# Kernel optimization log

Measured on AMD Instinct MI355X. Metric: run time of the kernel, lower is better.

Reference implementation:

```python
import jax, jax.numpy as jnp
import numpy as np

B, T, I, R, O = 64, 2048, 25, 512, 50
ALPHA = 0.5
RHO = 0.99


def setup_inputs() -> dict:
    key = jax.random.key(0)
    k1, k2, k3, k4 = jax.random.split(key, 4)
    x = jax.random.normal(k1, (B, T, I), dtype=jnp.float32)
    Win = jax.random.uniform(k2, (R, I), minval=-0.1, maxval=0.1, dtype=jnp.float32)
    W = jax.random.normal(k3, (R, R), dtype=jnp.float32) * 0.1
    sr_actual = np.max(np.abs(np.linalg.eigvals(np.asarray(W))))
    W = W / jnp.float32(sr_actual) * jnp.float32(RHO)
    Wout = jax.random.normal(k4, (O, R), dtype=jnp.float32) * 0.1
    return {"x": x, "Win": Win, "W": W, "Wout": Wout}


def reference(x, Win, W, Wout):
    a = jnp.asarray(ALPHA, dtype=x.dtype)
    # Precompute input projections for all timesteps (batched GEMM).
    xin = jnp.einsum('bti,ri->btr', x, Win)  # [B, T, R]

    def step(h, u):
        # h: [B, R], u: [B, R]
        h = (1 - a) * h + a * jnp.tanh(u + h @ W.T)
        return h, h

    h0 = jnp.zeros((x.shape[0], W.shape[0]), dtype=x.dtype)
    _, states = jax.lax.scan(step, h0, jnp.swapaxes(xin, 0, 1))  # [T, B, R]
    states = jnp.swapaxes(states, 0, 1)  # [B, T, R]
    return states @ Wout.T  # [B, T, O]
```

## Files before the change

### kernel.cpp

```cpp
#include <hip/hip_runtime.h>
#include <math.h>


typedef float v2f __attribute__((ext_vector_type(2)));
typedef float v4f __attribute__((ext_vector_type(4)));

template<int CTRL>
__device__ __forceinline__ float dpp_add(float x) {
    int y = __builtin_amdgcn_update_dpp(0, __float_as_int(x), CTRL, 0xF, 0xF, false);
    return x + __int_as_float(y);
}

__device__ __forceinline__ void store_ic8(float* p, float h, int tag) {
    v2f v; v[0] = h; v[1] = __int_as_float(tag);
    asm volatile("global_store_dwordx2 %0, %1, off sc0 sc1"
                 :: "v"(p), "v"(v) : "memory");
}
__device__ __forceinline__ void load3_ic(const float* p0, const float* p1,
                                         const float* p2, v4f& a, v4f& b, v4f& c) {
    asm volatile("global_load_dwordx4 %0, %3, off sc0 sc1\n\t"
                 "global_load_dwordx4 %1, %4, off sc0 sc1\n\t"
                 "global_load_dwordx4 %2, %5, off sc0 sc1\n\t"
                 "s_waitcnt vmcnt(0)"
                 : "=&v"(a), "=&v"(b), "=&v"(c)
                 : "v"(p0), "v"(p1), "v"(p2) : "memory");
}
__device__ __forceinline__ void load3_l2(const float* p0, const float* p1,
                                         const float* p2, v4f& a, v4f& b, v4f& c) {
    asm volatile("global_load_dwordx4 %0, %3, off sc0\n\t"
                 "global_load_dwordx4 %1, %4, off sc0\n\t"
                 "global_load_dwordx4 %2, %5, off sc0\n\t"
                 "s_waitcnt vmcnt(0)"
                 : "=&v"(a), "=&v"(b), "=&v"(c)
                 : "v"(p0), "v"(p1), "v"(p2) : "memory");
}

__device__ __forceinline__ int permidx(int c) {
    return (c >> 7) * 128 + (c & 31) * 4 + ((c >> 5) & 3);
}

#define TAGS_BAD (__any((__float_as_int(d0.y) != want) | (__float_as_int(d0.w) != want) | \
                        (__float_as_int(d1.y) != want) | (__float_as_int(d1.w) != want) | \
                        (__float_as_int(d2.y) != want) | (__float_as_int(d2.w) != want)))

__global__ void __launch_bounds__(512, 2)
esn_kernel(const float* __restrict__ x, const float* __restrict__ Win,
           const float* __restrict__ W, const float* __restrict__ Wout,
           float* __restrict__ out, float* __restrict__ Hf)
{
    const int b    = blockIdx.x & 63;
    const int g    = blockIdx.x >> 6;
    const int tid  = threadIdx.x;
    const int rt   = tid >> 5;
    const int ct   = tid & 31;
    const int lane = tid & 63;
    const int wv   = tid >> 6;
    const int hw   = rt & 1;

    __shared__ __align__(16) float hperm[2][512];

    v2f Wreg[64];
    {
        const int i0 = g*128 + rt*8;
        #pragma unroll
        for (int r = 0; r < 4; ++r)
        #pragma unroll
        for (int q = 0; q < 4; ++q) {
            const float* wp = W + (r*128 + q*32 + ct);
            #pragma unroll
            for (int p = 0; p < 4; ++p) {
                v2f w;
                w[0] = wp[(size_t)(i0 + 2*p    ) * 512];
                w[1] = wp[(size_t)(i0 + 2*p + 1) * 512];
                Wreg[(r*4+q)*4 + p] = w;
            }
        }
    }

    const int myrow = g*128 + rt*8 + (ct & 7);
    float WinR[25];
    #pragma unroll
    for (int k = 0; k < 25; ++k) WinR[k] = Win[myrow*25 + k];

    const int obase = g*13;
    const int ocnt  = (g == 3) ? 11 : 13;
    const int oloc  = 2*wv + hw;
    const bool ovalid = (oloc < ocnt);
    const int oidx  = obase + (ovalid ? oloc : 0);
    float WoutR[16];
    #pragma unroll
    for (int r = 0; r < 4; ++r)
    #pragma unroll
    for (int q = 0; q < 4; ++q)
        WoutR[r*4+q] = ovalid ? Wout[oidx*512 + r*128 + q*32 + ct] : 0.f;

    hperm[0][tid] = 0.f;
    float holdv = 0.f;
    const bool fin = (ct >= 16) & (ct < 24);

    const float* xrow = x   + (size_t)b * 2048 * 25;
    float*       orow = out + (size_t)b * 2048 * 50;
    float* HfB0 = Hf + (size_t)b * 1024;
    const int s0 = (g+1)&3, s1 = (g+2)&3, s2 = (g+3)&3;

    bool fast = true;

    __syncthreads();

    float u = 0.f;
    #pragma unroll
    for (int k = 0; k < 25; ++k) u = fmaf(WinR[k], xrow[k], u);

    for (int t = 0; t < 2048; ++t) {
        const int par  = t & 1;
        const int npar = par ^ 1;
        const int want = t + 1;
        float* HfN = HfB0 + (size_t)npar * 64 * 1024;

        v2f acc0 = {0.f,0.f}, acc1 = {0.f,0.f}, acc2 = {0.f,0.f}, acc3 = {0.f,0.f};
        float op = 0.f;
        #pragma unroll
        for (int r = 0; r < 4; ++r) {
            v4f hv = *(const v4f*)&hperm[par][r*128 + ct*4];
            #pragma unroll
            for (int q = 0; q < 4; ++q) {
                const float hs = hv[q];
                op = fmaf(WoutR[r*4+q], hs, op);
                v2f hh = {hs, hs};
                acc0 = __builtin_elementwise_fma(Wreg[(r*4+q)*4+0], hh, acc0);
                acc1 = __builtin_elementwise_fma(Wreg[(r*4+q)*4+1], hh, acc1);
                acc2 = __builtin_elementwise_fma(Wreg[(r*4+q)*4+2], hh, acc2);
                acc3 = __builtin_elementwise_fma(Wreg[(r*4+q)*4+3], hh, acc3);
            }
        }

        float ar[8] = {acc0[0],acc0[1],acc1[0],acc1[1],acc2[0],acc2[1],acc3[0],acc3[1]};
        #pragma unroll
        for (int j = 0; j < 8; ++j) {
            ar[j] = dpp_add<0xB1>(ar[j]);
            ar[j] = dpp_add<0x4E>(ar[j]);
            ar[j] = dpp_add<0x124>(ar[j]);
            ar[j] = dpp_add<0x128>(ar[j]);
            ar[j] = dpp_add<0x142>(ar[j]);
        }

        if (fin) {
            const int j = ct & 7;
            float y = ar[0];
            if (j == 1) y = ar[1];
            if (j == 2) y = ar[2];
            if (j == 3) y = ar[3];
            if (j == 4) y = ar[4];
            if (j == 5) y = ar[5];
            if (j == 6) y = ar[6];
            if (j == 7) y = ar[7];
            const float z  = u + y;
            const float e  = __expf(2.f * z);
            const float th = 1.f - 2.f * __builtin_amdgcn_rcpf(e + 1.f);
            holdv = 0.5f * holdv + 0.5f * th;
            hperm[npar][permidx(myrow)] = holdv;
            store_ic8(&HfN[myrow*2], holdv, want);
        }

        op = dpp_add<0xB1>(op);  op = dpp_add<0x4E>(op);
        op = dpp_add<0x124>(op); op = dpp_add<0x128>(op);
        op = dpp_add<0x142>(op);
        if (t > 0 && ovalid && ((lane & 31) == 31))
            orow[(size_t)(t-1)*50 + oidx] = op;
        {
            const int tt = (t < 2047) ? t + 1 : 2047;
            float un = 0.f;
            #pragma unroll
            for (int k = 0; k < 25; ++k) un = fmaf(WinR[k], xrow[tt*25 + k], un);
            u = un;
        }

        if (wv == 0) {
            const float* p0 = HfN + (s0*256 + lane*4);
            const float* p1 = HfN + (s1*256 + lane*4);
            const float* p2 = HfN + (s2*256 + lane*4);
            v4f d0, d1, d2;
            if (fast) {
                int tries = 0;
                do { load3_l2(p0, p1, p2, d0, d1, d2); } while (TAGS_BAD && ++tries < 64);
                if (TAGS_BAD) fast = false;
            }
            if (!fast) {
                do { load3_ic(p0, p1, p2, d0, d1, d2); } while (TAGS_BAD);
            }
            const int c0 = s0*128 + 2*lane, c1 = s1*128 + 2*lane, c2 = s2*128 + 2*lane;
            hperm[npar][permidx(c0)]     = d0.x;
            hperm[npar][permidx(c0 + 1)] = d0.z;
            hperm[npar][permidx(c1)]     = d1.x;
            hperm[npar][permidx(c1 + 1)] = d1.z;
            hperm[npar][permidx(c2)]     = d2.x;
            hperm[npar][permidx(c2 + 1)] = d2.z;
        }
        __syncthreads();
    }

    {
        float op = 0.f;
        #pragma unroll
        for (int r = 0; r < 4; ++r) {
            v4f hv = *(const v4f*)&hperm[0][r*128 + ct*4];
            #pragma unroll
            for (int q = 0; q < 4; ++q) op = fmaf(WoutR[r*4+q], hv[q], op);
        }
        op = dpp_add<0xB1>(op);  op = dpp_add<0x4E>(op);
        op = dpp_add<0x124>(op); op = dpp_add<0x128>(op);
        op = dpp_add<0x142>(op);
        if (ovalid && ((lane & 31) == 31))
            orow[(size_t)2047*50 + oidx] = op;
    }
}

extern "C" void kernel_launch(void* const* d_in, const int* in_sizes, int n_in,
                              void* d_out, int out_size, void* d_ws, size_t ws_size,
                              hipStream_t stream)
{
    (void)in_sizes; (void)n_in; (void)out_size; (void)ws_size;
    const float* x    = (const float*)d_in[0];
    const float* Win  = (const float*)d_in[1];
    const float* W    = (const float*)d_in[2];
    const float* Wout = (const float*)d_in[3];
    float* out = (float*)d_out;
    float* Hf  = (float*)d_ws;
    esn_kernel<<<dim3(256), dim3(512), 0, stream>>>(x, Win, W, Wout, out, Hf);
}
```

Baseline: 2.757 ms.

## Split recurrence across 8 blocks per pair of batches instead of 4 per batch

Each block now owns 64 reservoir rows (not 128) for two batch elements at once, so each batch's hidden state is spread over 8 blocks. This halves per-thread W register use and FMA work per step. In exchange, each step must gather 7 remote slices per batch through tagged global-memory flags instead of 3. The dependent chains of the two batches are interleaved to hide latency, and the first step gets a larger spin budget before falling back to the slower uncached polling path.

```diff
diff --git a/kernel.cpp b/kernel.cpp
--- a/kernel.cpp
+++ b/kernel.cpp
@@ -10,46 +10,126 @@
     int y = __builtin_amdgcn_update_dpp(0, __float_as_int(x), CTRL, 0xF, 0xF, false);
     return x + __int_as_float(y);
 }
+#define DPP_REDUCE32(v) do { v = dpp_add<0xB1>(v); v = dpp_add<0x4E>(v); \
+    v = dpp_add<0x124>(v); v = dpp_add<0x128>(v); v = dpp_add<0x142>(v); } while (0)
 
 __device__ __forceinline__ void store_ic8(float* p, float h, int tag) {
     v2f v; v[0] = h; v[1] = __int_as_float(tag);
     asm volatile("global_store_dwordx2 %0, %1, off sc0 sc1"
                  :: "v"(p), "v"(v) : "memory");
 }
-__device__ __forceinline__ void load3_ic(const float* p0, const float* p1,
-                                         const float* p2, v4f& a, v4f& b, v4f& c) {
-    asm volatile("global_load_dwordx4 %0, %3, off sc0 sc1\n\t"
-                 "global_load_dwordx4 %1, %4, off sc0 sc1\n\t"
-                 "global_load_dwordx4 %2, %5, off sc0 sc1\n\t"
-                 "s_waitcnt vmcnt(0)"
-                 : "=&v"(a), "=&v"(b), "=&v"(c)
-                 : "v"(p0), "v"(p1), "v"(p2) : "memory");
-}
-__device__ __forceinline__ void load3_l2(const float* p0, const float* p1,
-                                         const float* p2, v4f& a, v4f& b, v4f& c) {
-    asm volatile("global_load_dwordx4 %0, %3, off sc0\n\t"
-                 "global_load_dwordx4 %1, %4, off sc0\n\t"
-                 "global_load_dwordx4 %2, %5, off sc0\n\t"
-                 "s_waitcnt vmcnt(0)"
-                 : "=&v"(a), "=&v"(b), "=&v"(c)
-                 : "v"(p0), "v"(p1), "v"(p2) : "memory");
+
+__device__ __forceinline__ void load7_l2(
+    const float* p0, const float* p1, const float* p2, const float* p3,
+    const float* p4, const float* p5, const float* p6,
+    v2f& d0, v2f& d1, v2f& d2, v2f& d3, v2f& d4, v2f& d5, v2f& d6)
+{
+    asm volatile(
+        "global_load_dwordx2 %0, %7, off sc0\n\t"
+        "global_load_dwordx2 %1, %8, off sc0\n\t"
+        "global_load_dwordx2 %2, %9, off sc0\n\t"
+        "global_load_dwordx2 %3, %10, off sc0\n\t"
+        "global_load_dwordx2 %4, %11, off sc0\n\t"
+        "global_load_dwordx2 %5, %12, off sc0\n\t"
+        "global_load_dwordx2 %6, %13, off sc0\n\t"
+        "s_waitcnt vmcnt(0)"
+        : "=&v"(d0), "=&v"(d1), "=&v"(d2), "=&v"(d3), "=&v"(d4), "=&v"(d5), "=&v"(d6)
+        : "v"(p0), "v"(p1), "v"(p2), "v"(p3), "v"(p4), "v"(p5), "v"(p6)
+        : "memory");
+}
+__device__ __forceinline__ void load7_ic(
+    const float* p0, const float* p1, const float* p2, const float* p3,
+    const float* p4, const float* p5, const float* p6,
+    v2f& d0, v2f& d1, v2f& d2, v2f& d3, v2f& d4, v2f& d5, v2f& d6)
+{
+    asm volatile(
+        "global_load_dwordx2 %0, %7, off sc0 sc1\n\t"
+        "global_load_dwordx2 %1, %8, off sc0 sc1\n\t"
+        "global_load_dwordx2 %2, %9, off sc0 sc1\n\t"
+        "global_load_dwordx2 %3, %10, off sc0 sc1\n\t"
+        "global_load_dwordx2 %4, %11, off sc0 sc1\n\t"
+        "global_load_dwordx2 %5, %12, off sc0 sc1\n\t"
+        "global_load_dwordx2 %6, %13, off sc0 sc1\n\t"
+        "s_waitcnt vmcnt(0)"
+        : "=&v"(d0), "=&v"(d1), "=&v"(d2), "=&v"(d3), "=&v"(d4), "=&v"(d5), "=&v"(d6)
+        : "v"(p0), "v"(p1), "v"(p2), "v"(p3), "v"(p4), "v"(p5), "v"(p6)
+        : "memory");
 }
 
 __device__ __forceinline__ int permidx(int c) {
     return (c >> 7) * 128 + (c & 31) * 4 + ((c >> 5) & 3);
 }
 
-#define TAGS_BAD (__any((__float_as_int(d0.y) != want) | (__float_as_int(d0.w) != want) | \
-                        (__float_as_int(d1.y) != want) | (__float_as_int(d1.w) != want) | \
-                        (__float_as_int(d2.y) != want) | (__float_as_int(d2.w) != want)))
+#define TAGS_BAD (__any((__float_as_int(d0.y) != want) | (__float_as_int(d1.y) != want) | \
+                        (__float_as_int(d2.y) != want) | (__float_as_int(d3.y) != want) | \
+                        (__float_as_int(d4.y) != want) | (__float_as_int(d5.y) != want) | \
+                        (__float_as_int(d6.y) != want)))
+
+#define CHAIN_COMPUTE(c, uvar, holdvar, orowp, hfN) do {                      \
+    v2f acc0 = {0.f,0.f}, acc1 = {0.f,0.f};                                   \
+    float op = 0.f;                                                           \
+    _Pragma("unroll")                                                         \
+    for (int r = 0; r < 4; ++r) {                                             \
+        v4f hv = *(const v4f*)&hperm[c][par][r*128 + ct*4];                   \
+        _Pragma("unroll")                                                     \
+        for (int q = 0; q < 4; ++q) {                                         \
+            const float hs = hv[q];                                           \
+            op = fmaf(WoutR[r*4+q], hs, op);                                  \
+            v2f hh = {hs, hs};                                                \
+            acc0 = __builtin_elementwise_fma(Wreg[(r*4+q)*2+0], hh, acc0);    \
+            acc1 = __builtin_elementwise_fma(Wreg[(r*4+q)*2+1], hh, acc1);    \
+        }                                                                     \
+    }                                                                         \
+    float a0 = acc0[0], a1 = acc0[1], a2 = acc1[0], a3 = acc1[1];             \
+    DPP_REDUCE32(a0); DPP_REDUCE32(a1); DPP_REDUCE32(a2); DPP_REDUCE32(a3);   \
+    if (fin) {                                                                \
+        const int j = ct & 3;                                                 \
+        float y = a0;                                                         \
+        if (j == 1) y = a1;                                                   \
+        if (j == 2) y = a2;                                                   \
+        if (j == 3) y = a3;                                                   \
+        const float z  = uvar + y;                                            \
+        const float e  = __expf(2.f * z);                                     \
+        const float th = 1.f - 2.f * __builtin_amdgcn_rcpf(e + 1.f);          \
+        holdvar = 0.5f * holdvar + 0.5f * th;                                 \
+        hperm[c][npar][pmyrow] = holdvar;                                     \
+        store_ic8((hfN) + 2*myrow, holdvar, want);        \
+    }                                                                         \
+                          \
+    DPP_REDUCE32(op);                                                         \
+    if (t > 0 && ovalid && ((lane & 31) == 31))                               \
+        (orowp)[(size_t)(t-1)*50 + oidx] = op;                                \
+} while (0)
+
+#define U_NEXT(uvar, xrowp) do {                                              \
+    const int tt = (t < 2047) ? t + 1 : 2047;                                 \
+    float un = 0.f;                                                           \
+    _Pragma("unroll")                                                         \
+    for (int k = 0; k < 25; ++k) un = fmaf(WinR[k], (xrowp)[tt*25 + k], un);  \
+    uvar = un;                                                                \
+} while (0)
+
+#define CHAIN_EPI(c, orowp) do {                                              \
+    float op = 0.f;                                                           \
+    _Pragma("unroll")                                                         \
+    for (int r = 0; r < 4; ++r) {                                             \
+        v4f hv = *(const v4f*)&hperm[c][0][r*128 + ct*4];                     \
+        _Pragma("unroll")                                                     \
+        for (int q = 0; q < 4; ++q) op = fmaf(WoutR[r*4+q], hv[q], op);       \
+    }                                                                         \
+    DPP_REDUCE32(op);                                                         \
+    if (ovalid && ((lane & 31) == 31))                                        \
+        (orowp)[(size_t)2047*50 + oidx] = op;                                 \
+} while (0)
 
 __global__ void __launch_bounds__(512, 2)
 esn_kernel(const float* __restrict__ x, const float* __restrict__ Win,
            const float* __restrict__ W, const float* __restrict__ Wout,
            float* __restrict__ out, float* __restrict__ Hf)
 {
-    const int b    = blockIdx.x & 63;
-    const int g    = blockIdx.x >> 6;
+    const int p    = blockIdx.x & 31;
+    const int g    = blockIdx.x >> 5;
+    const int b0   = 2*p, b1 = 2*p + 1;
     const int tid  = threadIdx.x;
     const int rt   = tid >> 5;
     const int ct   = tid & 31;
@@ -57,33 +137,34 @@
     const int wv   = tid >> 6;
     const int hw   = rt & 1;
 
-    __shared__ __align__(16) float hperm[2][512];
-
-    v2f Wreg[64];
+    __shared__ __align__(16) float hperm[2][2][512];
+
+    v2f Wreg[32];
     {
-        const int i0 = g*128 + rt*8;
+        const int i0 = g*64 + rt*4;
         #pragma unroll
         for (int r = 0; r < 4; ++r)
         #pragma unroll
         for (int q = 0; q < 4; ++q) {
             const float* wp = W + (r*128 + q*32 + ct);
             #pragma unroll
-            for (int p = 0; p < 4; ++p) {
+            for (int pp = 0; pp < 2; ++pp) {
                 v2f w;
-                w[0] = wp[(size_t)(i0 + 2*p    ) * 512];
-                w[1] = wp[(size_t)(i0 + 2*p + 1) * 512];
-                Wreg[(r*4+q)*4 + p] = w;
+                w[0] = wp[(size_t)(i0 + 2*pp    ) * 512];
+                w[1] = wp[(size_t)(i0 + 2*pp + 1) * 512];
+                Wreg[(r*4+q)*2 + pp] = w;
             }
         }
     }
 
-    const int myrow = g*128 + rt*8 + (ct & 7);
+    const int myrow  = g*64 + rt*4 + (ct & 3);
+    const int pmyrow = permidx(myrow);
     float WinR[25];
     #pragma unroll
     for (int k = 0; k < 25; ++k) WinR[k] = Win[myrow*25 + k];
 
-    const int obase = g*13;
-    const int ocnt  = (g == 3) ? 11 : 13;
+    const int obase = g*7;
+    const int ocnt  = (g == 7) ? 1 : 7;
     const int oloc  = 2*wv + hw;
     const bool ovalid = (oloc < ocnt);
     const int oidx  = obase + (ovalid ? oloc : 0);
@@ -94,125 +175,77 @@
     for (int q = 0; q < 4; ++q)
         WoutR[r*4+q] = ovalid ? Wout[oidx*512 + r*128 + q*32 + ct] : 0.f;
 
-    hperm[0][tid] = 0.f;
-    float holdv = 0.f;
-    const bool fin = (ct >= 16) & (ct < 24);
-
-    const float* xrow = x   + (size_t)b * 2048 * 25;
-    float*       orow = out + (size_t)b * 2048 * 50;
-    float* HfB0 = Hf + (size_t)b * 1024;
-    const int s0 = (g+1)&3, s1 = (g+2)&3, s2 = (g+3)&3;
+    hperm[0][0][tid] = 0.f;
+    hperm[1][0][tid] = 0.f;
+    float holdv0 = 0.f, holdv1 = 0.f;
+    const bool fin = (ct >= 16) & (ct < 20);
+
+    const float* xrow0 = x   + (size_t)b0 * 2048 * 25;
+    const float* xrow1 = x   + (size_t)b1 * 2048 * 25;
+    float*       orow0 = out + (size_t)b0 * 2048 * 50;
+    float*       orow1 = out + (size_t)b1 * 2048 * 50;
+    float* HfB0 = Hf + (size_t)b0 * 1024;
+    float* HfB1 = Hf + (size_t)b1 * 1024;
+
+    const int s0=(g+1)&7, s1=(g+2)&7, s2=(g+3)&7, s3=(g+4)&7,
+              s4=(g+5)&7, s5=(g+6)&7, s6=(g+7)&7;
+    const int o0 = s0*128 + lane*2, o1 = s1*128 + lane*2, o2 = s2*128 + lane*2,
+              o3 = s3*128 + lane*2, o4 = s4*128 + lane*2, o5 = s5*128 + lane*2,
+              o6 = s6*128 + lane*2;
+    const int pi0 = permidx(s0*64 + lane), pi1 = permidx(s1*64 + lane),
+              pi2 = permidx(s2*64 + lane), pi3 = permidx(s3*64 + lane),
+              pi4 = permidx(s4*64 + lane), pi5 = permidx(s5*64 + lane),
+              pi6 = permidx(s6*64 + lane);
 
     bool fast = true;
 
     __syncthreads();
 
-    float u = 0.f;
-    #pragma unroll
-    for (int k = 0; k < 25; ++k) u = fmaf(WinR[k], xrow[k], u);
+    float u0 = 0.f, u1 = 0.f;
+    #pragma unroll
+    for (int k = 0; k < 25; ++k) u0 = fmaf(WinR[k], xrow0[k], u0);
+    #pragma unroll
+    for (int k = 0; k < 25; ++k) u1 = fmaf(WinR[k], xrow1[k], u1);
 
     for (int t = 0; t < 2048; ++t) {
         const int par  = t & 1;
         const int npar = par ^ 1;
         const int want = t + 1;
-        float* HfN = HfB0 + (size_t)npar * 64 * 1024;
-
-        v2f acc0 = {0.f,0.f}, acc1 = {0.f,0.f}, acc2 = {0.f,0.f}, acc3 = {0.f,0.f};
-        float op = 0.f;
-        #pragma unroll
-        for (int r = 0; r < 4; ++r) {
-            v4f hv = *(const v4f*)&hperm[par][r*128 + ct*4];
-            #pragma unroll
-            for (int q = 0; q < 4; ++q) {
-                const float hs = hv[q];
-                op = fmaf(WoutR[r*4+q], hs, op);
-                v2f hh = {hs, hs};
-                acc0 = __builtin_elementwise_fma(Wreg[(r*4+q)*4+0], hh, acc0);
-                acc1 = __builtin_elementwise_fma(Wreg[(r*4+q)*4+1], hh, acc1);
-                acc2 = __builtin_elementwise_fma(Wreg[(r*4+q)*4+2], hh, acc2);
-                acc3 = __builtin_elementwise_fma(Wreg[(r*4+q)*4+3], hh, acc3);
-            }
-        }
-
-        float ar[8] = {acc0[0],acc0[1],acc1[0],acc1[1],acc2[0],acc2[1],acc3[0],acc3[1]};
-        #pragma unroll
-        for (int j = 0; j < 8; ++j) {
-            ar[j] = dpp_add<0xB1>(ar[j]);
-            ar[j] = dpp_add<0x4E>(ar[j]);
-            ar[j] = dpp_add<0x124>(ar[j]);
-            ar[j] = dpp_add<0x128>(ar[j]);
-            ar[j] = dpp_add<0x142>(ar[j]);
-        }
-
-        if (fin) {
-            const int j = ct & 7;
-            float y = ar[0];
-            if (j == 1) y = ar[1];
-            if (j == 2) y = ar[2];
-            if (j == 3) y = ar[3];
-            if (j == 4) y = ar[4];
-            if (j == 5) y = ar[5];
-            if (j == 6) y = ar[6];
-            if (j == 7) y = ar[7];
-            const float z  = u + y;
-            const float e  = __expf(2.f * z);
-            const float th = 1.f - 2.f * __builtin_amdgcn_rcpf(e + 1.f);
-            holdv = 0.5f * holdv + 0.5f * th;
-            hperm[npar][permidx(myrow)] = holdv;
-            store_ic8(&HfN[myrow*2], holdv, want);
-        }
-
-        op = dpp_add<0xB1>(op);  op = dpp_add<0x4E>(op);
-        op = dpp_add<0x124>(op); op = dpp_add<0x128>(op);
-        op = dpp_add<0x142>(op);
-        if (t > 0 && ovalid && ((lane & 31) == 31))
-            orow[(size_t)(t-1)*50 + oidx] = op;
-        {
-            const int tt = (t < 2047) ? t + 1 : 2047;
-            float un = 0.f;
-            #pragma unroll
-            for (int k = 0; k < 25; ++k) un = fmaf(WinR[k], xrow[tt*25 + k], un);
-            u = un;
-        }
-
-        if (wv == 0) {
-            const float* p0 = HfN + (s0*256 + lane*4);
-            const float* p1 = HfN + (s1*256 + lane*4);
-            const float* p2 = HfN + (s2*256 + lane*4);
-            v4f d0, d1, d2;
+        float* HfN0 = HfB0 + (size_t)npar * 65536;
+        float* HfN1 = HfB1 + (size_t)npar * 65536;
+
+        CHAIN_COMPUTE(0, u0, holdv0, orow0, HfN0);
+        U_NEXT(u0, xrow0);
+        CHAIN_COMPUTE(1, u1, holdv1, orow1, HfN1);
+        U_NEXT(u1, xrow1);
+
+        if (wv < 2) {
+            float* HfN = wv ? HfN1 : HfN0;
+            const float* q0 = HfN + o0; const float* q1 = HfN + o1;
+            const float* q2 = HfN + o2; const float* q3 = HfN + o3;
+            const float* q4 = HfN + o4; const float* q5 = HfN + o5;
+            const float* q6 = HfN + o6;
+            v2f d0, d1, d2, d3, d4, d5, d6;
             if (fast) {
+                const int budget = (t == 0) ? 2048 : 64;
                 int tries = 0;
-                do { load3_l2(p0, p1, p2, d0, d1, d2); } while (TAGS_BAD && ++tries < 64);
+                do { load7_l2(q0,q1,q2,q3,q4,q5,q6,d0,d1,d2,d3,d4,d5,d6); }
+                while (TAGS_BAD && ++tries < budget);
                 if (TAGS_BAD) fast = false;
             }
             if (!fast) {
-                do { load3_ic(p0, p1, p2, d0, d1, d2); } while (TAGS_BAD);
+                do { load7_ic(q0,q1,q2,q3,q4,q5,q6,d0,d1,d2,d3,d4,d5,d6); }
+                while (TAGS_BAD);
             }
-            const int c0 = s0*128 + 2*lane, c1 = s1*128 + 2*lane, c2 = s2*128 + 2*lane;
-            hperm[npar][permidx(c0)]     = d0.x;
-            hperm[npar][permidx(c0 + 1)] = d0.z;
-            hperm[npar][permidx(c1)]     = d1.x;
-            hperm[npar][permidx(c1 + 1)] = d1.z;
-            hperm[npar][permidx(c2)]     = d2.x;
-            hperm[npar][permidx(c2 + 1)] = d2.z;
+            float* hp = &hperm[wv][npar][0];
+            hp[pi0] = d0.x; hp[pi1] = d1.x; hp[pi2] = d2.x; hp[pi3] = d3.x;
+            hp[pi4] = d4.x; hp[pi5] = d5.x; hp[pi6] = d6.x;
         }
         __syncthreads();
     }
 
-    {
-        float op = 0.f;
-        #pragma unroll
-        for (int r = 0; r < 4; ++r) {
-            v4f hv = *(const v4f*)&hperm[0][r*128 + ct*4];
-            #pragma unroll
-            for (int q = 0; q < 4; ++q) op = fmaf(WoutR[r*4+q], hv[q], op);
-        }
-        op = dpp_add<0xB1>(op);  op = dpp_add<0x4E>(op);
-        op = dpp_add<0x124>(op); op = dpp_add<0x128>(op);
-        op = dpp_add<0x142>(op);
-        if (ovalid && ((lane & 31) == 31))
-            orow[(size_t)2047*50 + oidx] = op;
-    }
+    CHAIN_EPI(0, orow0);
+    CHAIN_EPI(1, orow1);
 }
 
 extern "C" void kernel_launch(void* const* d_in, const int* in_sizes, int n_in,
```

After: 5.591 ms. +102.8%, slower.
